# Performance work log

Hardware: AMD Instinct MI355X
Metric: run time of the kernel (lower is better)

## Reference

```python
import jax, jax.numpy as jnp
import numpy as np

N = 20000      # nodes
E = 640000     # edges (before self loops)
IN = 256       # in_channels == out_channels (forced by classifier size 4*in)
H1, C1 = 8, 16   # conv1: heads=8, out=16 -> concat 128
H2, C2 = 1, 256  # conv2: heads=1, out=out_channels
B = 4096       # article pairs
NEG_SLOPE = 0.2  # PyG GATv2Conv default negative_slope


def setup_inputs() -> dict:
    key = jax.random.key(0)
    ks = jax.random.split(key, 24)
    s = 0.05
    inp = {
        "gnn_x": jax.random.normal(ks[0], (N, IN), jnp.float32),
        "vanilla_x": jax.random.normal(ks[1], (N, IN), jnp.float32),
        "edge_src": jax.random.randint(ks[2], (E,), 0, N, jnp.int32),
        "edge_dst": jax.random.randint(ks[3], (E,), 0, N, jnp.int32),
        "a1_idx": jax.random.randint(ks[4], (B,), 0, N, jnp.int64),
        "a2_idx": jax.random.randint(ks[5], (B,), 0, N, jnp.int64),
        # conv1 params (lin_l, lin_r, att, bias)
        "Wl1": jax.random.normal(ks[6], (IN, H1 * C1), jnp.float32) * s,
        "bl1": jnp.zeros((H1 * C1,), jnp.float32),
        "Wr1": jax.random.normal(ks[7], (IN, H1 * C1), jnp.float32) * s,
        "br1": jnp.zeros((H1 * C1,), jnp.float32),
        "att1": jax.random.normal(ks[8], (H1, C1), jnp.float32) * s,
        "bias1": jnp.zeros((H1 * C1,), jnp.float32),
        # conv2 params
        "Wl2": jax.random.normal(ks[9], (H1 * C1, H2 * C2), jnp.float32) * s,
        "bl2": jnp.zeros((H2 * C2,), jnp.float32),
        "Wr2": jax.random.normal(ks[10], (H1 * C1, H2 * C2), jnp.float32) * s,
        "br2": jnp.zeros((H2 * C2,), jnp.float32),
        "att2": jax.random.normal(ks[11], (H2, C2), jnp.float32) * s,
        "bias2": jnp.zeros((H2 * C2,), jnp.float32),
        # classifier
        "Wc": jax.random.normal(ks[12], (4 * IN, 1), jnp.float32) * s,
        "bc": jnp.zeros((1,), jnp.float32),
    }
    return inp


def _gatv2_layer(x, src, dst, Wl, bl, Wr, br, att, bias):
    """GATv2Conv: x_l = lin_l(x)[src], x_r = lin_r(x)[dst];
    e = att . leaky_relu(x_l + x_r); segment softmax over dst; scatter-add x_l*alpha."""
    n = x.shape[0]
    h, c = att.shape
    xl = (x @ Wl + bl).reshape(n, h, c)
    xr = (x @ Wr + br).reshape(n, h, c)
    # per-edge attention logits [E, H]
    e = jnp.einsum('ehc,hc->eh', jax.nn.leaky_relu(xl[src] + xr[dst], NEG_SLOPE), att)
    # segment softmax over destination nodes (self loops guarantee non-empty segments)
    emax = jax.ops.segment_max(e, dst, num_segments=n)
    ex = jnp.exp(e - emax[dst])
    denom = jax.ops.segment_sum(ex, dst, num_segments=n)
    alpha = ex / denom[dst]                      # [E, H]
    out = jax.ops.segment_sum(alpha[:, :, None] * xl[src], dst, num_segments=n)  # [N,H,C]
    return out.reshape(n, h * c) + bias          # concat=True (heads=1 identical)


def reference(gnn_x, vanilla_x, Wl1, bl1, Wr1, br1, att1, bias1,
              Wl2, bl2, Wr2, br2, att2, bias2, Wc, bc,
              edge_src, edge_dst, a1_idx, a2_idx):
    n = gnn_x.shape[0]
    loops = jnp.arange(n, dtype=edge_src.dtype)
    src = jnp.concatenate([edge_src, loops])     # PyG add_self_loops=True
    dst = jnp.concatenate([edge_dst, loops])
    x = _gatv2_layer(gnn_x, src, dst, Wl1, bl1, Wr1, br1, att1, bias1)
    x = jax.nn.relu(x)
    x = _gatv2_layer(x, src, dst, Wl2, bl2, Wr2, br2, att2, bias2)
    combined = jnp.concatenate(
        [vanilla_x[a1_idx], vanilla_x[a2_idx], x[a1_idx], x[a2_idx]], axis=1)  # [B, 4*IN]
    logits = combined @ Wc + bc                  # [B, 1]
    return logits
```

## Files before the change

### kernel.cpp

```cpp
#include <hip/hip_runtime.h>
#include <math.h>

#define N_NODES 20000
#define M_PAD   20032
#define E_EDGES 640000
#define ET (E_EDGES + N_NODES)
#define IN_CH 256
#define D1 128
#define D2 256
#define BPAIRS 4096
#define NEG 0.2f
#define LOG2E 1.4426950408889634f

#define XCONV_BLOCKS 5008
#define WCONV_BLOCKS 512
#define HIST_BLOCKS  ((ET + 255) / 256)

#if __has_builtin(__builtin_amdgcn_exp2f)
#define EXP2F(x) __builtin_amdgcn_exp2f(x)
#else
#define EXP2F(x) exp2f(x)
#endif

typedef __bf16 bf16x8 __attribute__((ext_vector_type(8)));
typedef float  f32x4  __attribute__((ext_vector_type(4)));

__device__ __forceinline__ unsigned short f2b(float f) {
    unsigned int u = __float_as_uint(f);
    unsigned int r = u + 0x7FFFu + ((u >> 16) & 1u);
    return (unsigned short)(r >> 16);
}
__device__ __forceinline__ float b2f(unsigned short h) {
    return __uint_as_float(((unsigned int)h) << 16);
}
__device__ __forceinline__ float lrelu(float s) { return fmaxf(s, NEG * s); }

__device__ __forceinline__ void unpack8(uint4 u, float* v) {
    v[0] = __uint_as_float(u.x << 16); v[1] = __uint_as_float(u.x & 0xFFFF0000u);
    v[2] = __uint_as_float(u.y << 16); v[3] = __uint_as_float(u.y & 0xFFFF0000u);
    v[4] = __uint_as_float(u.z << 16); v[5] = __uint_as_float(u.z & 0xFFFF0000u);
    v[6] = __uint_as_float(u.w << 16); v[7] = __uint_as_float(u.w & 0xFFFF0000u);
}
__device__ __forceinline__ void unpack4(uint2 u, float* v) {
    v[0] = __uint_as_float(u.x << 16); v[1] = __uint_as_float(u.x & 0xFFFF0000u);
    v[2] = __uint_as_float(u.y << 16); v[3] = __uint_as_float(u.y & 0xFFFF0000u);
}


__global__ void prep_kernel(
        const float* __restrict__ gnn_x,
        const float* __restrict__ Wl1, const float* __restrict__ Wr1,
        const float* __restrict__ Wl2, const float* __restrict__ Wr2,
        const int* __restrict__ edge_dst,
        unsigned short* __restrict__ xb,
        unsigned short* __restrict__ wt1l, unsigned short* __restrict__ wt1r,
        unsigned short* __restrict__ wt2l, unsigned short* __restrict__ wt2r,
        int* __restrict__ count, int* __restrict__ rank) {
    int bid = blockIdx.x;
    if (bid < XCONV_BLOCKS) {
        int e0 = (bid * 256 + threadIdx.x) * 4;
        int row = e0 >> 8;
        ushort4 o;
        if (row < N_NODES) {
            float4 v = *(const float4*)(gnn_x + e0);
            o.x = f2b(v.x); o.y = f2b(v.y); o.z = f2b(v.z); o.w = f2b(v.w);
        } else {
            o.x = o.y = o.z = o.w = 0;
        }
        *(ushort4*)(xb + e0) = o;
    } else if (bid < XCONV_BLOCKS + WCONV_BLOCKS) {
        int idx = (bid - XCONV_BLOCKS) * 256 + threadIdx.x;
        int seg = idx >> 15;
        int r = idx & 32767;
        const float* W;
        unsigned short* Wt;
        int k, n, K;
        if (seg < 2) {
            W = seg ? Wr1 : Wl1; Wt = seg ? wt1r : wt1l;
            k = r >> 7; n = r & 127; K = IN_CH;
        } else {
            W = (seg & 1) ? Wr2 : Wl2; Wt = (seg & 1) ? wt2r : wt2l;
            k = r >> 8; n = r & 255; K = D1;
        }
        Wt[n * K + k] = f2b(W[r]);
    } else {
        int e = (bid - XCONV_BLOCKS - WCONV_BLOCKS) * 256 + threadIdx.x;
        if (e >= ET) return;
        int dst = (e < E_EDGES) ? edge_dst[e] : (e - E_EDGES);
        rank[e] = atomicAdd(&count[dst], 1);
    }
}


__global__ __launch_bounds__(1024) void scan_kernel(const int* __restrict__ count,
                                                    int* __restrict__ offsets) {
    const int PER = 20;
    int t = threadIdx.x;
    int base = t * PER;
    int local[PER];
    int sum = 0;
#pragma unroll
    for (int i = 0; i < PER; i++) {
        int idx = base + i;
        int v = (idx < N_NODES) ? count[idx] : 0;
        local[i] = sum;
        sum += v;
    }
    int lane = t & 63, wave = t >> 6;
    int s = sum;
#pragma unroll
    for (int off = 1; off < 64; off <<= 1) {
        int x = __shfl_up(s, off);
        if (lane >= off) s += x;
    }
    __shared__ int wsum[16];
    __shared__ int wpre[16];
    if (lane == 63) wsum[wave] = s;
    __syncthreads();
    if (t == 0) {
        int acc = 0;
        for (int w = 0; w < 16; w++) { wpre[w] = acc; acc += wsum[w]; }
        offsets[N_NODES] = acc;
    }
    __syncthreads();
    int thread_excl = wpre[wave] + (s - sum);
#pragma unroll
    for (int i = 0; i < PER; i++) {
        int idx = base + i;
        if (idx < N_NODES) offsets[idx] = thread_excl + local[i];
    }
}

__global__ void scatter_kernel(const int* __restrict__ edge_src,
                               const int* __restrict__ edge_dst,
                               const int* __restrict__ rank,
                               const int* __restrict__ offsets,
                               int* __restrict__ sorted_src) {
    int e = blockIdx.x * blockDim.x + threadIdx.x;
    if (e >= ET) return;
    int dst = (e < E_EDGES) ? edge_dst[e] : (e - E_EDGES);
    int src = (e < E_EDGES) ? edge_src[e] : (e - E_EDGES);
    sorted_src[offsets[dst] + rank[e]] = src;
}


template <int K>
__global__ __launch_bounds__(256) void dual_gemm_mfma_kernel(
        const unsigned short* __restrict__ A,
        const unsigned short* __restrict__ Wtl,
        const unsigned short* __restrict__ Wtr,
        const float* __restrict__ bl, const float* __restrict__ br,
        unsigned short* __restrict__ Yl, unsigned short* __restrict__ Yr,
        int M, int NOUT) {
    int wave = threadIdx.x >> 6;
    int lane = threadIdx.x & 63;
    int row0 = blockIdx.x * 64;
    int col0 = (blockIdx.y * 4 + wave) * 16;
    int rsub = lane & 15;
    int koff = (lane >> 4) * 8;

    const unsigned short* ap  = A   + (size_t)(row0 + rsub) * K + koff;
    const unsigned short* bpl = Wtl + (size_t)(col0 + rsub) * K + koff;
    const unsigned short* bpr = Wtr + (size_t)(col0 + rsub) * K + koff;

    f32x4 l0 = {0.f, 0.f, 0.f, 0.f};
    f32x4 l1 = l0, l2 = l0, l3 = l0, r0 = l0, r1 = l0, r2 = l0, r3 = l0;

#pragma unroll
    for (int kb = 0; kb < K; kb += 32) {
        bf16x8 bfl = *(const bf16x8*)(bpl + kb);
        bf16x8 bfr = *(const bf16x8*)(bpr + kb);
        bf16x8 a0 = *(const bf16x8*)(ap + kb);
        bf16x8 a1 = *(const bf16x8*)(ap + 16 * K + kb);
        bf16x8 a2 = *(const bf16x8*)(ap + 32 * K + kb);
        bf16x8 a3 = *(const bf16x8*)(ap + 48 * K + kb);
        l0 = __builtin_amdgcn_mfma_f32_16x16x32_bf16(a0, bfl, l0, 0, 0, 0);
        r0 = __builtin_amdgcn_mfma_f32_16x16x32_bf16(a0, bfr, r0, 0, 0, 0);
        l1 = __builtin_amdgcn_mfma_f32_16x16x32_bf16(a1, bfl, l1, 0, 0, 0);
        r1 = __builtin_amdgcn_mfma_f32_16x16x32_bf16(a1, bfr, r1, 0, 0, 0);
        l2 = __builtin_amdgcn_mfma_f32_16x16x32_bf16(a2, bfl, l2, 0, 0, 0);
        r2 = __builtin_amdgcn_mfma_f32_16x16x32_bf16(a2, bfr, r2, 0, 0, 0);
        l3 = __builtin_amdgcn_mfma_f32_16x16x32_bf16(a3, bfl, l3, 0, 0, 0);
        r3 = __builtin_amdgcn_mfma_f32_16x16x32_bf16(a3, bfr, r3, 0, 0, 0);
    }

    int colg = col0 + rsub;
    float bvl = bl[colg];
    float bvr = br[colg];
    int rbase = row0 + (lane >> 4) * 4;
#pragma unroll
    for (int t = 0; t < 4; t++) {
        f32x4 al = (t == 0) ? l0 : (t == 1) ? l1 : (t == 2) ? l2 : l3;
        f32x4 ar = (t == 0) ? r0 : (t == 1) ? r1 : (t == 2) ? r2 : r3;
#pragma unroll
        for (int r = 0; r < 4; r++) {
            int row = rbase + t * 16 + r;
            if (row < M) {
                Yl[(size_t)row * NOUT + colg] = f2b(al[r] + bvl);
                Yr[(size_t)row * NOUT + colg] = f2b(ar[r] + bvr);
            }
        }
    }
}


__global__ __launch_bounds__(256) void aggregate1_kernel(
        const unsigned short* __restrict__ xl1, const unsigned short* __restrict__ xr1,
        const float* __restrict__ att1, const float* __restrict__ bias1,
        const int* __restrict__ offsets, const int* __restrict__ sorted_src,
        unsigned short* __restrict__ x1) {
    int wave = threadIdx.x >> 6;
    int lane = threadIdx.x & 63;
    int half = lane >> 5;
    int hl = lane & 31;
    int dst = blockIdx.x * 4 + wave;
    if (dst >= M_PAD) return;
    int c0 = hl * 4;
    if (dst >= N_NODES) {
        if (half == 0) {
            uint2 z; z.x = 0; z.y = 0;
            *(uint2*)(x1 + (size_t)dst * D1 + c0) = z;
        }
        return;
    }

    float xr[4], att[4];
    unpack4(*(const uint2*)(xr1 + (size_t)dst * D1 + c0), xr);
#pragma unroll
    for (int j = 0; j < 4; j++) att[j] = att1[c0 + j] * LOG2E;
    int beg = offsets[dst], end = offsets[dst + 1];

    float l = 0.f;
    float A0 = 0.f, A1 = 0.f, A2 = 0.f, A3 = 0.f;
    int i = beg;
    for (; i + 4 <= end; i += 4) {
        int sA = sorted_src[i + half];
        int sB = sorted_src[i + 2 + half];
        float vA[4], vB[4];
        unpack4(*(const uint2*)(xl1 + (size_t)sA * D1 + c0), vA);
        unpack4(*(const uint2*)(xl1 + (size_t)sB * D1 + c0), vB);
        float pA = att[0] * lrelu(vA[0] + xr[0]) + att[1] * lrelu(vA[1] + xr[1])
                 + att[2] * lrelu(vA[2] + xr[2]) + att[3] * lrelu(vA[3] + xr[3]);
        float pB = att[0] * lrelu(vB[0] + xr[0]) + att[1] * lrelu(vB[1] + xr[1])
                 + att[2] * lrelu(vB[2] + xr[2]) + att[3] * lrelu(vB[3] + xr[3]);
        pA += __shfl_xor(pA, 1); pB += __shfl_xor(pB, 1);
        pA += __shfl_xor(pA, 2); pB += __shfl_xor(pB, 2);
        float wA = EXP2F(pA), wB = EXP2F(pB);
        l += wA + wB;
        A0 += wA * vA[0] + wB * vB[0];
        A1 += wA * vA[1] + wB * vB[1];
        A2 += wA * vA[2] + wB * vB[2];
        A3 += wA * vA[3] + wB * vB[3];
    }
    for (; i + 2 <= end; i += 2) {
        int sA = sorted_src[i + half];
        float vA[4];
        unpack4(*(const uint2*)(xl1 + (size_t)sA * D1 + c0), vA);
        float pA = att[0] * lrelu(vA[0] + xr[0]) + att[1] * lrelu(vA[1] + xr[1])
                 + att[2] * lrelu(vA[2] + xr[2]) + att[3] * lrelu(vA[3] + xr[3]);
        pA += __shfl_xor(pA, 1);
        pA += __shfl_xor(pA, 2);
        float wA = EXP2F(pA);
        l += wA;
        A0 += wA * vA[0]; A1 += wA * vA[1]; A2 += wA * vA[2]; A3 += wA * vA[3];
    }
    if (i < end && half == 0) {
        int sA = sorted_src[i];
        float vA[4];
        unpack4(*(const uint2*)(xl1 + (size_t)sA * D1 + c0), vA);
        float pA = att[0] * lrelu(vA[0] + xr[0]) + att[1] * lrelu(vA[1] + xr[1])
                 + att[2] * lrelu(vA[2] + xr[2]) + att[3] * lrelu(vA[3] + xr[3]);
        pA += __shfl_xor(pA, 1);
        pA += __shfl_xor(pA, 2);
        float wA = EXP2F(pA);
        l += wA;
        A0 += wA * vA[0]; A1 += wA * vA[1]; A2 += wA * vA[2]; A3 += wA * vA[3];
    }
    l  += __shfl_xor(l, 32);
    A0 += __shfl_xor(A0, 32);
    A1 += __shfl_xor(A1, 32);
    A2 += __shfl_xor(A2, 32);
    A3 += __shfl_xor(A3, 32);
    if (half == 0) {
        float inv = 1.f / l;
        unsigned short o0 = f2b(fmaxf(A0 * inv + bias1[c0 + 0], 0.f));
        unsigned short o1 = f2b(fmaxf(A1 * inv + bias1[c0 + 1], 0.f));
        unsigned short o2 = f2b(fmaxf(A2 * inv + bias1[c0 + 2], 0.f));
        unsigned short o3 = f2b(fmaxf(A3 * inv + bias1[c0 + 3], 0.f));
        uint2 o;
        o.x = (unsigned int)o0 | ((unsigned int)o1 << 16);
        o.y = (unsigned int)o2 | ((unsigned int)o3 << 16);
        *(uint2*)(x1 + (size_t)dst * D1 + c0) = o;
    }
}


__global__ __launch_bounds__(256) void aggregate2_kernel(
        const unsigned short* __restrict__ xl2, const unsigned short* __restrict__ xr2,
        const float* __restrict__ att2, const float* __restrict__ bias2,
        const int* __restrict__ offsets, const int* __restrict__ sorted_src,
        float* __restrict__ x2) {
    int wave = threadIdx.x >> 6;
    int lane = threadIdx.x & 63;
    int half = lane >> 5;
    int hl = lane & 31;
    int dst = blockIdx.x * 4 + wave;
    if (dst >= N_NODES) return;
    int c0 = hl * 8;

    float xr[8], att[8];
    unpack8(*(const uint4*)(xr2 + (size_t)dst * D2 + c0), xr);
#pragma unroll
    for (int j = 0; j < 8; j++) att[j] = att2[c0 + j] * LOG2E;
    int beg = offsets[dst], end = offsets[dst + 1];

    float l = 0.f;
    float acc[8];
#pragma unroll
    for (int j = 0; j < 8; j++) acc[j] = 0.f;

    int i = beg;
    for (; i + 4 <= end; i += 4) {
        int sA = sorted_src[i + half];
        int sB = sorted_src[i + 2 + half];
        float vA[8], vB[8];
        unpack8(*(const uint4*)(xl2 + (size_t)sA * D2 + c0), vA);
        unpack8(*(const uint4*)(xl2 + (size_t)sB * D2 + c0), vB);
        float pA = 0.f, pB = 0.f;
#pragma unroll
        for (int j = 0; j < 8; j++) pA = fmaf(att[j], lrelu(vA[j] + xr[j]), pA);
#pragma unroll
        for (int j = 0; j < 8; j++) pB = fmaf(att[j], lrelu(vB[j] + xr[j]), pB);
        pA += __shfl_xor(pA, 1);  pB += __shfl_xor(pB, 1);
        pA += __shfl_xor(pA, 2);  pB += __shfl_xor(pB, 2);
        pA += __shfl_xor(pA, 4);  pB += __shfl_xor(pB, 4);
        pA += __shfl_xor(pA, 8);  pB += __shfl_xor(pB, 8);
        pA += __shfl_xor(pA, 16); pB += __shfl_xor(pB, 16);
        float wA = EXP2F(pA), wB = EXP2F(pB);
        l += wA + wB;
#pragma unroll
        for (int j = 0; j < 8; j++) acc[j] += wA * vA[j] + wB * vB[j];
    }
    for (; i + 2 <= end; i += 2) {
        int sA = sorted_src[i + half];
        float vA[8];
        unpack8(*(const uint4*)(xl2 + (size_t)sA * D2 + c0), vA);
        float pA = 0.f;
#pragma unroll
        for (int j = 0; j < 8; j++) pA = fmaf(att[j], lrelu(vA[j] + xr[j]), pA);
        pA += __shfl_xor(pA, 1);
        pA += __shfl_xor(pA, 2);
        pA += __shfl_xor(pA, 4);
        pA += __shfl_xor(pA, 8);
        pA += __shfl_xor(pA, 16);
        float wA = EXP2F(pA);
        l += wA;
#pragma unroll
        for (int j = 0; j < 8; j++) acc[j] += wA * vA[j];
    }
    if (i < end && half == 0) {
        int sA = sorted_src[i];
        float vA[8];
        unpack8(*(const uint4*)(xl2 + (size_t)sA * D2 + c0), vA);
        float pA = 0.f;
#pragma unroll
        for (int j = 0; j < 8; j++) pA = fmaf(att[j], lrelu(vA[j] + xr[j]), pA);
        pA += __shfl_xor(pA, 1);
        pA += __shfl_xor(pA, 2);
        pA += __shfl_xor(pA, 4);
        pA += __shfl_xor(pA, 8);
        pA += __shfl_xor(pA, 16);
        float wA = EXP2F(pA);
        l += wA;
#pragma unroll
        for (int j = 0; j < 8; j++) acc[j] += wA * vA[j];
    }
    l += __shfl_xor(l, 32);
#pragma unroll
    for (int j = 0; j < 8; j++) acc[j] += __shfl_xor(acc[j], 32);
    if (half == 0) {
        float inv = 1.f / l;
        float4 o0, o1;
        o0.x = acc[0] * inv + bias2[c0 + 0];
        o0.y = acc[1] * inv + bias2[c0 + 1];
        o0.z = acc[2] * inv + bias2[c0 + 2];
        o0.w = acc[3] * inv + bias2[c0 + 3];
        o1.x = acc[4] * inv + bias2[c0 + 4];
        o1.y = acc[5] * inv + bias2[c0 + 5];
        o1.z = acc[6] * inv + bias2[c0 + 6];
        o1.w = acc[7] * inv + bias2[c0 + 7];
        *(float4*)(x2 + (size_t)dst * D2 + c0) = o0;
        *(float4*)(x2 + (size_t)dst * D2 + c0 + 4) = o1;
    }
}


__global__ __launch_bounds__(256) void classifier_kernel(
        const float* __restrict__ vanilla_x, const float* __restrict__ x2,
        const int* __restrict__ a1_raw, const int* __restrict__ a2_raw,
        const float* __restrict__ Wc, const float* __restrict__ bc,
        float* __restrict__ out) {
    int b = blockIdx.x;
    int t = threadIdx.x;

    __shared__ int stride_s;
    if (t == 0) {
        bool i64 = true;
        for (int i = 1; i < 63; i += 2) i64 = i64 && (a1_raw[i] == 0);
        stride_s = i64 ? 2 : 1;
    }
    __syncthreads();
    int stride = stride_s;
    int a1 = a1_raw[(long)b * stride];
    int a2 = a2_raw[(long)b * stride];

    float s = vanilla_x[a1 * IN_CH + t] * Wc[t]
            + vanilla_x[a2 * IN_CH + t] * Wc[IN_CH + t]
            + x2[a1 * D2 + t] * Wc[2 * IN_CH + t]
            + x2[a2 * D2 + t] * Wc[3 * IN_CH + t];
    s += __shfl_xor(s, 1);
    s += __shfl_xor(s, 2);
    s += __shfl_xor(s, 4);
    s += __shfl_xor(s, 8);
    s += __shfl_xor(s, 16);
    s += __shfl_xor(s, 32);
    __shared__ float part[4];
    if ((t & 63) == 0) part[t >> 6] = s;
    __syncthreads();
    if (t == 0) out[b] = part[0] + part[1] + part[2] + part[3] + bc[0];
}


extern "C" void kernel_launch(void* const* d_in, const int* in_sizes, int n_in,
                              void* d_out, int out_size, void* d_ws, size_t ws_size,
                              hipStream_t stream) {
    const float* gnn_x     = (const float*)d_in[0];
    const float* vanilla_x = (const float*)d_in[1];
    const int*   edge_src  = (const int*)d_in[2];
    const int*   edge_dst  = (const int*)d_in[3];
    const int*   a1_idx    = (const int*)d_in[4];
    const int*   a2_idx    = (const int*)d_in[5];
    const float* Wl1   = (const float*)d_in[6];
    const float* bl1   = (const float*)d_in[7];
    const float* Wr1   = (const float*)d_in[8];
    const float* br1   = (const float*)d_in[9];
    const float* att1  = (const float*)d_in[10];
    const float* bias1 = (const float*)d_in[11];
    const float* Wl2   = (const float*)d_in[12];
    const float* bl2   = (const float*)d_in[13];
    const float* Wr2   = (const float*)d_in[14];
    const float* br2   = (const float*)d_in[15];
    const float* att2  = (const float*)d_in[16];
    const float* bias2 = (const float*)d_in[17];
    const float* Wc    = (const float*)d_in[18];
    const float* bc    = (const float*)d_in[19];
    float* out = (float*)d_out;

    char* p = (char*)d_ws;
    unsigned short* xb   = (unsigned short*)p; p += (size_t)M_PAD * IN_CH * 2;
    unsigned short* x1b  = (unsigned short*)p; p += (size_t)M_PAD * D1 * 2;
    unsigned short* xl1b = (unsigned short*)p; p += (size_t)N_NODES * D1 * 2;
    unsigned short* xr1b = (unsigned short*)p; p += (size_t)N_NODES * D1 * 2;
    unsigned short* xl2b = (unsigned short*)p; p += (size_t)N_NODES * D2 * 2;
    unsigned short* xr2b = (unsigned short*)p; p += (size_t)N_NODES * D2 * 2;
    unsigned short* wt1l = (unsigned short*)p; p += (size_t)D1 * IN_CH * 2;
    unsigned short* wt1r = (unsigned short*)p; p += (size_t)D1 * IN_CH * 2;
    unsigned short* wt2l = (unsigned short*)p; p += (size_t)D2 * D1 * 2;
    unsigned short* wt2r = (unsigned short*)p; p += (size_t)D2 * D1 * 2;
    float* x2 = (float*)p; p += (size_t)N_NODES * D2 * 4;
    int* count      = (int*)p; p += (size_t)N_NODES * 4;
    int* offsets    = (int*)p; p += (size_t)(N_NODES + 4) * 4;
    int* rank       = (int*)p; p += (size_t)ET * 4;
    int* sorted_src = (int*)p; p += (size_t)ET * 4;

    hipMemsetAsync(count, 0, (size_t)N_NODES * sizeof(int), stream);

    prep_kernel<<<XCONV_BLOCKS + WCONV_BLOCKS + HIST_BLOCKS, 256, 0, stream>>>(
        gnn_x, Wl1, Wr1, Wl2, Wr2, edge_dst,
        xb, wt1l, wt1r, wt2l, wt2r, count, rank);
    scan_kernel<<<1, 1024, 0, stream>>>(count, offsets);
    scatter_kernel<<<HIST_BLOCKS, 256, 0, stream>>>(
        edge_src, edge_dst, rank, offsets, sorted_src);

    dim3 g1(M_PAD / 64, D1 / 64);
    dual_gemm_mfma_kernel<IN_CH><<<g1, 256, 0, stream>>>(
        xb, wt1l, wt1r, bl1, br1, xl1b, xr1b, N_NODES, D1);
    aggregate1_kernel<<<M_PAD / 4, 256, 0, stream>>>(
        xl1b, xr1b, att1, bias1, offsets, sorted_src, x1b);

    dim3 g2(M_PAD / 64, D2 / 64);
    dual_gemm_mfma_kernel<D1><<<g2, 256, 0, stream>>>(
        x1b, wt2l, wt2r, bl2, br2, xl2b, xr2b, N_NODES, D2);
    aggregate2_kernel<<<(N_NODES + 3) / 4, 256, 0, stream>>>(
        xl2b, xr2b, att2, bias2, offsets, sorted_src, x2);

    classifier_kernel<<<BPAIRS, 256, 0, stream>>>(
        vanilla_x, x2, a1_idx, a2_idx, Wc, bc, out);
}
```

Before: 298.8 us.

## Software-pipeline edge gathers and pack math in GAT aggregation kernels

Both aggregation kernels now prefetch the next group of neighbor rows while computing on the current group. The tail loops are replaced by masked lanes whose weight is forced to zero. Layer 1 now has each lane handle 8 channels with 16-byte loads, so four edges are processed per iteration. The math is rewritten with 2-wide float vectors so the compiler can emit packed FP32 instructions. The aim is to hide gather latency and cut instruction count, at the cost of more registers and redundant clamped loads for partial groups.

```diff
diff --git a/kernel.cpp b/kernel.cpp
--- a/kernel.cpp
+++ b/kernel.cpp
@@ -24,26 +24,21 @@
 
 typedef __bf16 bf16x8 __attribute__((ext_vector_type(8)));
 typedef float  f32x4  __attribute__((ext_vector_type(4)));
+typedef float  f32x2  __attribute__((ext_vector_type(2)));
 
 __device__ __forceinline__ unsigned short f2b(float f) {
     unsigned int u = __float_as_uint(f);
     unsigned int r = u + 0x7FFFu + ((u >> 16) & 1u);
     return (unsigned short)(r >> 16);
 }
-__device__ __forceinline__ float b2f(unsigned short h) {
-    return __uint_as_float(((unsigned int)h) << 16);
-}
-__device__ __forceinline__ float lrelu(float s) { return fmaxf(s, NEG * s); }
-
-__device__ __forceinline__ void unpack8(uint4 u, float* v) {
-    v[0] = __uint_as_float(u.x << 16); v[1] = __uint_as_float(u.x & 0xFFFF0000u);
-    v[2] = __uint_as_float(u.y << 16); v[3] = __uint_as_float(u.y & 0xFFFF0000u);
-    v[4] = __uint_as_float(u.z << 16); v[5] = __uint_as_float(u.z & 0xFFFF0000u);
-    v[6] = __uint_as_float(u.w << 16); v[7] = __uint_as_float(u.w & 0xFFFF0000u);
-}
-__device__ __forceinline__ void unpack4(uint2 u, float* v) {
-    v[0] = __uint_as_float(u.x << 16); v[1] = __uint_as_float(u.x & 0xFFFF0000u);
-    v[2] = __uint_as_float(u.y << 16); v[3] = __uint_as_float(u.y & 0xFFFF0000u);
+__device__ __forceinline__ f32x2 up2(unsigned int u) {
+    f32x2 r;
+    r.x = __uint_as_float(u << 16);
+    r.y = __uint_as_float(u & 0xFFFF0000u);
+    return r;
+}
+__device__ __forceinline__ f32x2 lrelu2(f32x2 s) {
+    return __builtin_elementwise_max(s, s * NEG);
 }
 
 
@@ -211,86 +206,89 @@
         unsigned short* __restrict__ x1) {
     int wave = threadIdx.x >> 6;
     int lane = threadIdx.x & 63;
-    int half = lane >> 5;
-    int hl = lane & 31;
+    int q = lane >> 4;
+    int ql = lane & 15;
     int dst = blockIdx.x * 4 + wave;
     if (dst >= M_PAD) return;
-    int c0 = hl * 4;
+    int c0 = ql * 8;
     if (dst >= N_NODES) {
-        if (half == 0) {
-            uint2 z; z.x = 0; z.y = 0;
-            *(uint2*)(x1 + (size_t)dst * D1 + c0) = z;
+        if (q == 0) {
+            uint4 z; z.x = z.y = z.z = z.w = 0;
+            *(uint4*)(x1 + (size_t)dst * D1 + c0) = z;
         }
         return;
     }
 
-    float xr[4], att[4];
-    unpack4(*(const uint2*)(xr1 + (size_t)dst * D1 + c0), xr);
-#pragma unroll
-    for (int j = 0; j < 4; j++) att[j] = att1[c0 + j] * LOG2E;
+    uint4 xu = *(const uint4*)(xr1 + (size_t)dst * D1 + c0);
+    f32x2 xr[4] = {up2(xu.x), up2(xu.y), up2(xu.z), up2(xu.w)};
+    float4 aa0 = *(const float4*)(att1 + c0);
+    float4 aa1 = *(const float4*)(att1 + c0 + 4);
+    f32x2 att[4];
+    att[0].x = aa0.x * LOG2E; att[0].y = aa0.y * LOG2E;
+    att[1].x = aa0.z * LOG2E; att[1].y = aa0.w * LOG2E;
+    att[2].x = aa1.x * LOG2E; att[2].y = aa1.y * LOG2E;
+    att[3].x = aa1.z * LOG2E; att[3].y = aa1.w * LOG2E;
+
     int beg = offsets[dst], end = offsets[dst + 1];
+    const unsigned short* base = xl1 + c0;
 
     float l = 0.f;
-    float A0 = 0.f, A1 = 0.f, A2 = 0.f, A3 = 0.f;
+    f32x2 acc[4] = {{0.f,0.f},{0.f,0.f},{0.f,0.f},{0.f,0.f}};
+
     int i = beg;
-    for (; i + 4 <= end; i += 4) {
-        int sA = sorted_src[i + half];
-        int sB = sorted_src[i + 2 + half];
-        float vA[4], vB[4];
-        unpack4(*(const uint2*)(xl1 + (size_t)sA * D1 + c0), vA);
-        unpack4(*(const uint2*)(xl1 + (size_t)sB * D1 + c0), vB);
-        float pA = att[0] * lrelu(vA[0] + xr[0]) + att[1] * lrelu(vA[1] + xr[1])
-                 + att[2] * lrelu(vA[2] + xr[2]) + att[3] * lrelu(vA[3] + xr[3]);
-        float pB = att[0] * lrelu(vB[0] + xr[0]) + att[1] * lrelu(vB[1] + xr[1])
-                 + att[2] * lrelu(vB[2] + xr[2]) + att[3] * lrelu(vB[3] + xr[3]);
-        pA += __shfl_xor(pA, 1); pB += __shfl_xor(pB, 1);
-        pA += __shfl_xor(pA, 2); pB += __shfl_xor(pB, 2);
-        float wA = EXP2F(pA), wB = EXP2F(pB);
-        l += wA + wB;
-        A0 += wA * vA[0] + wB * vB[0];
-        A1 += wA * vA[1] + wB * vB[1];
-        A2 += wA * vA[2] + wB * vB[2];
-        A3 += wA * vA[3] + wB * vB[3];
-    }
-    for (; i + 2 <= end; i += 2) {
-        int sA = sorted_src[i + half];
-        float vA[4];
-        unpack4(*(const uint2*)(xl1 + (size_t)sA * D1 + c0), vA);
-        float pA = att[0] * lrelu(vA[0] + xr[0]) + att[1] * lrelu(vA[1] + xr[1])
-                 + att[2] * lrelu(vA[2] + xr[2]) + att[3] * lrelu(vA[3] + xr[3]);
-        pA += __shfl_xor(pA, 1);
-        pA += __shfl_xor(pA, 2);
-        float wA = EXP2F(pA);
-        l += wA;
-        A0 += wA * vA[0]; A1 += wA * vA[1]; A2 += wA * vA[2]; A3 += wA * vA[3];
-    }
-    if (i < end && half == 0) {
-        int sA = sorted_src[i];
-        float vA[4];
-        unpack4(*(const uint2*)(xl1 + (size_t)sA * D1 + c0), vA);
-        float pA = att[0] * lrelu(vA[0] + xr[0]) + att[1] * lrelu(vA[1] + xr[1])
-                 + att[2] * lrelu(vA[2] + xr[2]) + att[3] * lrelu(vA[3] + xr[3]);
-        pA += __shfl_xor(pA, 1);
-        pA += __shfl_xor(pA, 2);
-        float wA = EXP2F(pA);
-        l += wA;
-        A0 += wA * vA[0]; A1 += wA * vA[1]; A2 += wA * vA[2]; A3 += wA * vA[3];
-    }
-    l  += __shfl_xor(l, 32);
-    A0 += __shfl_xor(A0, 32);
-    A1 += __shfl_xor(A1, 32);
-    A2 += __shfl_xor(A2, 32);
-    A3 += __shfl_xor(A3, 32);
-    if (half == 0) {
+    int s0 = sorted_src[min(i + q, end - 1)];
+    uint4 g0 = *(const uint4*)(base + (size_t)s0 * D1);
+    while (true) {
+        int inext = i + 4;
+        bool more = inext < end;
+        uint4 g1;
+        if (more) {
+            int s1 = sorted_src[min(inext + q, end - 1)];
+            g1 = *(const uint4*)(base + (size_t)s1 * D1);
+        }
+        bool act = (i + q) < end;
+        f32x2 v0 = up2(g0.x), v1 = up2(g0.y), v2 = up2(g0.z), v3 = up2(g0.w);
+        f32x2 p2 = att[0] * lrelu2(v0 + xr[0]);
+        p2 += att[1] * lrelu2(v1 + xr[1]);
+        p2 += att[2] * lrelu2(v2 + xr[2]);
+        p2 += att[3] * lrelu2(v3 + xr[3]);
+        float p = p2.x + p2.y;
+        p += __shfl_xor(p, 1);
+        float w = act ? EXP2F(p) : 0.f;
+        l += w;
+        acc[0] += w * v0; acc[1] += w * v1; acc[2] += w * v2; acc[3] += w * v3;
+        if (!more) break;
+        i = inext; g0 = g1;
+    }
+    l += __shfl_xor(l, 16);
+    l += __shfl_xor(l, 32);
+#pragma unroll
+    for (int j = 0; j < 4; j++) {
+        f32x2 t;
+        t.x = __shfl_xor(acc[j].x, 16); t.y = __shfl_xor(acc[j].y, 16);
+        acc[j] += t;
+        t.x = __shfl_xor(acc[j].x, 32); t.y = __shfl_xor(acc[j].y, 32);
+        acc[j] += t;
+    }
+    if (q == 0) {
         float inv = 1.f / l;
-        unsigned short o0 = f2b(fmaxf(A0 * inv + bias1[c0 + 0], 0.f));
-        unsigned short o1 = f2b(fmaxf(A1 * inv + bias1[c0 + 1], 0.f));
-        unsigned short o2 = f2b(fmaxf(A2 * inv + bias1[c0 + 2], 0.f));
-        unsigned short o3 = f2b(fmaxf(A3 * inv + bias1[c0 + 3], 0.f));
-        uint2 o;
-        o.x = (unsigned int)o0 | ((unsigned int)o1 << 16);
-        o.y = (unsigned int)o2 | ((unsigned int)o3 << 16);
-        *(uint2*)(x1 + (size_t)dst * D1 + c0) = o;
+        float4 bb0 = *(const float4*)(bias1 + c0);
+        float4 bb1 = *(const float4*)(bias1 + c0 + 4);
+        unsigned short o[8];
+        o[0] = f2b(fmaxf(acc[0].x * inv + bb0.x, 0.f));
+        o[1] = f2b(fmaxf(acc[0].y * inv + bb0.y, 0.f));
+        o[2] = f2b(fmaxf(acc[1].x * inv + bb0.z, 0.f));
+        o[3] = f2b(fmaxf(acc[1].y * inv + bb0.w, 0.f));
+        o[4] = f2b(fmaxf(acc[2].x * inv + bb1.x, 0.f));
+        o[5] = f2b(fmaxf(acc[2].y * inv + bb1.y, 0.f));
+        o[6] = f2b(fmaxf(acc[3].x * inv + bb1.z, 0.f));
+        o[7] = f2b(fmaxf(acc[3].y * inv + bb1.w, 0.f));
+        uint4 ov;
+        ov.x = (unsigned int)o[0] | ((unsigned int)o[1] << 16);
+        ov.y = (unsigned int)o[2] | ((unsigned int)o[3] << 16);
+        ov.z = (unsigned int)o[4] | ((unsigned int)o[5] << 16);
+        ov.w = (unsigned int)o[6] | ((unsigned int)o[7] << 16);
+        *(uint4*)(x1 + (size_t)dst * D1 + c0) = ov;
     }
 }
 
@@ -308,87 +306,87 @@
     if (dst >= N_NODES) return;
     int c0 = hl * 8;
 
-    float xr[8], att[8];
-    unpack8(*(const uint4*)(xr2 + (size_t)dst * D2 + c0), xr);
-#pragma unroll
-    for (int j = 0; j < 8; j++) att[j] = att2[c0 + j] * LOG2E;
+    uint4 xu = *(const uint4*)(xr2 + (size_t)dst * D2 + c0);
+    f32x2 xr[4] = {up2(xu.x), up2(xu.y), up2(xu.z), up2(xu.w)};
+    float4 aa0 = *(const float4*)(att2 + c0);
+    float4 aa1 = *(const float4*)(att2 + c0 + 4);
+    f32x2 att[4];
+    att[0].x = aa0.x * LOG2E; att[0].y = aa0.y * LOG2E;
+    att[1].x = aa0.z * LOG2E; att[1].y = aa0.w * LOG2E;
+    att[2].x = aa1.x * LOG2E; att[2].y = aa1.y * LOG2E;
+    att[3].x = aa1.z * LOG2E; att[3].y = aa1.w * LOG2E;
+
     int beg = offsets[dst], end = offsets[dst + 1];
+    const unsigned short* base = xl2 + c0;
 
     float l = 0.f;
-    float acc[8];
-#pragma unroll
-    for (int j = 0; j < 8; j++) acc[j] = 0.f;
+    f32x2 acc[4] = {{0.f,0.f},{0.f,0.f},{0.f,0.f},{0.f,0.f}};
 
     int i = beg;
-    for (; i + 4 <= end; i += 4) {
-        int sA = sorted_src[i + half];
-        int sB = sorted_src[i + 2 + half];
-        float vA[8], vB[8];
-        unpack8(*(const uint4*)(xl2 + (size_t)sA * D2 + c0), vA);
-        unpack8(*(const uint4*)(xl2 + (size_t)sB * D2 + c0), vB);
-        float pA = 0.f, pB = 0.f;
-#pragma unroll
-        for (int j = 0; j < 8; j++) pA = fmaf(att[j], lrelu(vA[j] + xr[j]), pA);
-#pragma unroll
-        for (int j = 0; j < 8; j++) pB = fmaf(att[j], lrelu(vB[j] + xr[j]), pB);
+    int sA = sorted_src[min(i + half, end - 1)];
+    int sB = sorted_src[min(i + 2 + half, end - 1)];
+    uint4 gA = *(const uint4*)(base + (size_t)sA * D2);
+    uint4 gB = *(const uint4*)(base + (size_t)sB * D2);
+    while (true) {
+        int inext = i + 4;
+        bool more = inext < end;
+        uint4 gA2, gB2;
+        if (more) {
+            int sA2 = sorted_src[min(inext + half, end - 1)];
+            int sB2 = sorted_src[min(inext + 2 + half, end - 1)];
+            gA2 = *(const uint4*)(base + (size_t)sA2 * D2);
+            gB2 = *(const uint4*)(base + (size_t)sB2 * D2);
+        }
+        bool actA = (i + half) < end;
+        bool actB = (i + 2 + half) < end;
+
+        f32x2 vA0 = up2(gA.x), vA1 = up2(gA.y), vA2 = up2(gA.z), vA3 = up2(gA.w);
+        f32x2 vB0 = up2(gB.x), vB1 = up2(gB.y), vB2 = up2(gB.z), vB3 = up2(gB.w);
+        f32x2 pA2 = att[0] * lrelu2(vA0 + xr[0]);
+        f32x2 pB2 = att[0] * lrelu2(vB0 + xr[0]);
+        pA2 += att[1] * lrelu2(vA1 + xr[1]);
+        pB2 += att[1] * lrelu2(vB1 + xr[1]);
+        pA2 += att[2] * lrelu2(vA2 + xr[2]);
+        pB2 += att[2] * lrelu2(vB2 + xr[2]);
+        pA2 += att[3] * lrelu2(vA3 + xr[3]);
+        pB2 += att[3] * lrelu2(vB3 + xr[3]);
+        float pA = pA2.x + pA2.y;
+        float pB = pB2.x + pB2.y;
         pA += __shfl_xor(pA, 1);  pB += __shfl_xor(pB, 1);
         pA += __shfl_xor(pA, 2);  pB += __shfl_xor(pB, 2);
         pA += __shfl_xor(pA, 4);  pB += __shfl_xor(pB, 4);
         pA += __shfl_xor(pA, 8);  pB += __shfl_xor(pB, 8);
         pA += __shfl_xor(pA, 16); pB += __shfl_xor(pB, 16);
-        float wA = EXP2F(pA), wB = EXP2F(pB);
+        float wA = actA ? EXP2F(pA) : 0.f;
+        float wB = actB ? EXP2F(pB) : 0.f;
         l += wA + wB;
-#pragma unroll
-        for (int j = 0; j < 8; j++) acc[j] += wA * vA[j] + wB * vB[j];
-    }
-    for (; i + 2 <= end; i += 2) {
-        int sA = sorted_src[i + half];
-        float vA[8];
-        unpack8(*(const uint4*)(xl2 + (size_t)sA * D2 + c0), vA);
-        float pA = 0.f;
-#pragma unroll
-        for (int j = 0; j < 8; j++) pA = fmaf(att[j], lrelu(vA[j] + xr[j]), pA);
-        pA += __shfl_xor(pA, 1);
-        pA += __shfl_xor(pA, 2);
-        pA += __shfl_xor(pA, 4);
-        pA += __shfl_xor(pA, 8);
-        pA += __shfl_xor(pA, 16);
-        float wA = EXP2F(pA);
-        l += wA;
-#pragma unroll
-        for (int j = 0; j < 8; j++) acc[j] += wA * vA[j];
-    }
-    if (i < end && half == 0) {
-        int sA = sorted_src[i];
-        float vA[8];
-        unpack8(*(const uint4*)(xl2 + (size_t)sA * D2 + c0), vA);
-        float pA = 0.f;
-#pragma unroll
-        for (int j = 0; j < 8; j++) pA = fmaf(att[j], lrelu(vA[j] + xr[j]), pA);
-        pA += __shfl_xor(pA, 1);
-        pA += __shfl_xor(pA, 2);
-        pA += __shfl_xor(pA, 4);
-        pA += __shfl_xor(pA, 8);
-        pA += __shfl_xor(pA, 16);
-        float wA = EXP2F(pA);
-        l += wA;
-#pragma unroll
-        for (int j = 0; j < 8; j++) acc[j] += wA * vA[j];
+        acc[0] += wA * vA0 + wB * vB0;
+        acc[1] += wA * vA1 + wB * vB1;
+        acc[2] += wA * vA2 + wB * vB2;
+        acc[3] += wA * vA3 + wB * vB3;
+        if (!more) break;
+        i = inext; gA = gA2; gB = gB2;
     }
     l += __shfl_xor(l, 32);
 #pragma unroll
-    for (int j = 0; j < 8; j++) acc[j] += __shfl_xor(acc[j], 32);
+    for (int j = 0; j < 4; j++) {
+        f32x2 t;
+        t.x = __shfl_xor(acc[j].x, 32); t.y = __shfl_xor(acc[j].y, 32);
+        acc[j] += t;
+    }
     if (half == 0) {
         float inv = 1.f / l;
+        float4 bb0 = *(const float4*)(bias2 + c0);
+        float4 bb1 = *(const float4*)(bias2 + c0 + 4);
         float4 o0, o1;
-        o0.x = acc[0] * inv + bias2[c0 + 0];
-        o0.y = acc[1] * inv + bias2[c0 + 1];
-        o0.z = acc[2] * inv + bias2[c0 + 2];
-        o0.w = acc[3] * inv + bias2[c0 + 3];
-        o1.x = acc[4] * inv + bias2[c0 + 4];
-        o1.y = acc[5] * inv + bias2[c0 + 5];
-        o1.z = acc[6] * inv + bias2[c0 + 6];
-        o1.w = acc[7] * inv + bias2[c0 + 7];
+        o0.x = acc[0].x * inv + bb0.x;
+        o0.y = acc[0].y * inv + bb0.y;
+        o0.z = acc[1].x * inv + bb0.z;
+        o0.w = acc[1].y * inv + bb0.w;
+        o1.x = acc[2].x * inv + bb1.x;
+        o1.y = acc[2].y * inv + bb1.y;
+        o1.z = acc[3].x * inv + bb1.z;
+        o1.w = acc[3].y * inv + bb1.w;
         *(float4*)(x2 + (size_t)dst * D2 + c0) = o0;
         *(float4*)(x2 + (size_t)dst * D2 + c0 + 4) = o1;
     }
```

Result: no change. 298.4 us (-0.1%).
